# Kernel optimization log

Measured on AMD Instinct MI355X. Metric: run time of the kernel, lower is better.

Reference implementation:

```python
import jax, jax.numpy as jnp
import numpy as np


def lstm_cell(x, h, c, Wih, Whh, b):
    # PyTorch LSTM gate order: i, f, g, o
    z = x @ Wih.T + h @ Whh.T + b
    i, f, g, o = jnp.split(z, 4, axis=-1)
    c = jax.nn.sigmoid(f) * c + jax.nn.sigmoid(i) * jnp.tanh(g)
    h = jax.nn.sigmoid(o) * jnp.tanh(c)
    return h, c


def run_dir(xs, Wih, Whh, b, reverse):
    # xs: [S, B, D_in] -> outputs [S, B, H], final (h, c)
    B = xs.shape[1]
    H = Whh.shape[1]
    init = (jnp.zeros((B, H), xs.dtype), jnp.zeros((B, H), xs.dtype))
    def step(carry, x):
        h, c = carry
        h, c = lstm_cell(x, h, c, Wih, Whh, b)
        return (h, c), h
    (h, c), ys = jax.lax.scan(step, init, xs, reverse=reverse)
    return ys, h, c


def _p(k, shape, scale=0.05):
    return jax.random.normal(k, shape, dtype=jnp.float32) * scale


def setup_inputs():
    V, E, H = 32000, 128, 256
    B, S, T = 32, 256, 64
    ks = jax.random.split(jax.random.key(0), 24)
    return {
        "src": jax.random.randint(ks[0], (B, S), 0, V),
        "tgt": jax.random.randint(ks[1], (B, T), 0, V),
        "emb": _p(ks[2], (V, E), 1.0),
        "enc_Wih_l0": _p(ks[3], (2, 4 * H, E)),
        "enc_Whh_l0": _p(ks[4], (2, 4 * H, H)),
        "enc_b_l0": _p(ks[5], (2, 4 * H)),
        "enc_Wih_l1": _p(ks[6], (2, 4 * H, 2 * H)),
        "enc_Whh_l1": _p(ks[7], (2, 4 * H, H)),
        "enc_b_l1": _p(ks[8], (2, 4 * H)),
        "dec_Wih0": _p(ks[9], (8 * H, E + 2 * H)),
        "dec_Whh0": _p(ks[10], (8 * H, 2 * H)),
        "dec_b0": _p(ks[11], (8 * H,)),
        "dec_Wih1": _p(ks[12], (8 * H, 2 * H)),
        "dec_Whh1": _p(ks[13], (8 * H, 2 * H)),
        "dec_b1": _p(ks[14], (8 * H,)),
        "attn_W1": _p(ks[15], (H, 4 * H)),
        "attn_b1": _p(ks[16], (H,)),
        "attn_W2": _p(ks[17], (1, H)),
        "attn_b2": _p(ks[18], (1,)),
        "out_W1": _p(ks[19], (H, 2 * H)),
        "out_b1": _p(ks[20], (H,)),
        "out_W2": _p(ks[21], (V, H)),
        "out_b2": _p(ks[22], (V,)),
    }


def reference(src, tgt, emb, enc_Wih_l0, enc_Whh_l0, enc_b_l0, enc_Wih_l1, enc_Whh_l1, enc_b_l1, dec_Wih0, dec_Whh0, dec_b0, dec_Wih1, dec_Whh1, dec_b1, attn_W1, attn_b1, attn_W2, attn_b2, out_W1, out_b1, out_W2, out_b2):
    # dropout layers are identity in eval mode
    H2 = dec_Whh0.shape[1]  # 2*hidden_dim = 512
    src_e = emb[src]                        # [B, S, E]
    tgt_e = emb[tgt]                        # [B, T, E]
    xs = jnp.swapaxes(src_e, 0, 1)          # [S, B, E]

    # 2-layer bidirectional encoder
    yf, hf0, cf0 = run_dir(xs, enc_Wih_l0[0], enc_Whh_l0[0], enc_b_l0[0], False)
    yb, hb0, cb0 = run_dir(xs, enc_Wih_l0[1], enc_Whh_l0[1], enc_b_l0[1], True)
    y0 = jnp.concatenate([yf, yb], axis=-1)  # [S, B, 2H]
    yf1, hf1, cf1 = run_dir(y0, enc_Wih_l1[0], enc_Whh_l1[0], enc_b_l1[0], False)
    yb1, hb1, cb1 = run_dir(y0, enc_Wih_l1[1], enc_Whh_l1[1], enc_b_l1[1], True)
    enc_out = jnp.swapaxes(jnp.concatenate([yf1, yb1], axis=-1), 0, 1)  # [B, S, 2H]

    # decoder init: per-layer concat of fwd/bwd final states (matches the view/transpose)
    h0 = jnp.concatenate([hf0, hb0], axis=-1)
    c0 = jnp.concatenate([cf0, cb0], axis=-1)
    h1 = jnp.concatenate([hf1, hb1], axis=-1)
    c1 = jnp.concatenate([cf1, cb1], axis=-1)

    # attention: Linear(4H, H) split into decoder-hidden part and encoder part
    W1_dec = attn_W1[:, :H2]
    W1_enc = attn_W1[:, H2:]
    enc_proj = jnp.einsum('bsd,hd->bsh', enc_out, W1_enc) + attn_b1  # precompute once

    dec_xs = jnp.swapaxes(tgt_e[:, :-1, :], 0, 1)  # [T-1, B, E]

    def step(carry, x_t):
        h0, c0, h1, c1 = carry
        e = jnp.tanh(enc_proj + (h1 @ W1_dec.T)[:, None, :])  # [B, S, H]
        scores = e @ attn_W2[0] + attn_b2[0]                  # [B, S]
        a = jax.nn.softmax(scores, axis=1)
        ctx = jnp.einsum('bs,bsd->bd', a, enc_out)            # [B, 2H]
        x = jnp.concatenate([x_t, ctx], axis=-1)              # [B, E+2H]
        h0, c0 = lstm_cell(x, h0, c0, dec_Wih0, dec_Whh0, dec_b0)
        h1, c1 = lstm_cell(h0, h1, c1, dec_Wih1, dec_Whh1, dec_b1)
        hid = jax.nn.relu(h1 @ out_W1.T + out_b1)
        logits = hid @ out_W2.T + out_b2                      # [B, V]
        return (h0, c0, h1, c1), logits

    _, ys = jax.lax.scan(step, (h0, c0, h1, c1), dec_xs)      # [T-1, B, V]
    return jnp.swapaxes(ys, 0, 1)                             # [B, T-1, V]
```

## Files before the change

kernel.cpp:

```cpp
#include <hip/hip_runtime.h>

#define BB_ 32
#define SS_ 256
#define TD_ 63
#define EE_ 128
#define VV_ 32000

typedef unsigned short u16;
typedef unsigned int u32;
typedef unsigned long long u64;
typedef __attribute__((ext_vector_type(8))) short short8v;
typedef __attribute__((ext_vector_type(4))) float f32x4;

__device__ __forceinline__ float sigf(float x){ return 1.0f/(1.0f+__expf(-x)); }
__device__ __forceinline__ float tanhf_fast(float x){ return 1.0f - 2.0f/(__expf(2.0f*x)+1.0f); }
__device__ __forceinline__ u16 f2bf(float f){
  unsigned u = __float_as_uint(f);
  u += 0x7fff + ((u >> 16) & 1);
  return (u16)(u >> 16);
}
__device__ __forceinline__ u32 packbf(float a, float b){
  return (u32)f2bf(a) | ((u32)f2bf(b) << 16);
}
__device__ __forceinline__ float bflo(u32 v){ return __uint_as_float(v << 16); }
__device__ __forceinline__ float bfhi(u32 v){ return __uint_as_float(v & 0xffff0000u); }

__device__ __forceinline__ u32 aldu(const u32* p){
  return __hip_atomic_load(p, __ATOMIC_RELAXED, __HIP_MEMORY_SCOPE_AGENT);
}
__device__ __forceinline__ u64 ald64u(const u32* p){
  return __hip_atomic_load((const u64*)p, __ATOMIC_RELAXED, __HIP_MEMORY_SCOPE_AGENT);
}
__device__ __forceinline__ void astu(u32* p, u32 v){
  __hip_atomic_store(p, v, __ATOMIC_RELAXED, __HIP_MEMORY_SCOPE_AGENT);
}
__device__ __forceinline__ float aldf(const float* p){
  return __hip_atomic_load(p, __ATOMIC_RELAXED, __HIP_MEMORY_SCOPE_AGENT);
}
__device__ __forceinline__ void astf(float* p, float v){
  __hip_atomic_store(p, v, __ATOMIC_RELAXED, __HIP_MEMORY_SCOPE_AGENT);
}
__device__ __forceinline__ void vdrain(){ asm volatile("s_waitcnt vmcnt(0)" ::: "memory"); }

__device__ __forceinline__ short8v mkfrag(u64 a, u64 b){
  union { u32 u[4]; short8v v; } c;
  c.u[0] = (u32)a; c.u[1] = (u32)(a >> 32);
  c.u[2] = (u32)b; c.u[3] = (u32)(b >> 32);
  return c.v;
}

#define OFF_Z        0u
#define OFF_Y0       16777216u
#define OFF_Y1       20971520u
#define OFF_ZPRE     25165824u
#define OFF_H1ALL    29294592u
#define OFF_SRCE     30326784u
#define OFF_TGTE     31375360u
#define OFF_EPROJ    31633408u
#define OFF_ENCA0    33730560u
#define OFF_ENCA1    33992704u
#define OFF_DECA     34254848u
#define OFF_ATP      36352000u
#define OFF_E0H      36417536u
#define OFF_E0C      36433920u
#define OFF_E1H      36450304u
#define OFF_E1C      36466688u
#define OFF_H0P      36483072u
#define OFF_H1P      36499456u
#define OFF_CTXP     36515840u
#define OFF_CTXS     36532224u
#define OFF_Y1P      36532288u
#define OFF_HEXA     38629440u
#define OFF_HEXB     38645824u
#define OFF_BARS     38662208u

__device__ __forceinline__ void icbar(unsigned* ctr, unsigned target){
  vdrain();
  __syncthreads();
  if (threadIdx.x == 0){
    __hip_atomic_fetch_add(ctr, 1u, __ATOMIC_RELAXED, __HIP_MEMORY_SCOPE_AGENT);
    while (__hip_atomic_load(ctr, __ATOMIC_RELAXED, __HIP_MEMORY_SCOPE_AGENT) < target)
      __builtin_amdgcn_s_sleep(1);
  }
  __syncthreads();
  asm volatile("" ::: "memory");
}

__device__ __forceinline__ void icbar3(unsigned* db, unsigned gen, bool isRoot){
  vdrain();
  __syncthreads();
  int tid = threadIdx.x;
  unsigned g = (unsigned)blockIdx.x & 15u;
  if (tid == 0)
    __hip_atomic_fetch_add(&db[g*32], 1u, __ATOMIC_RELAXED, __HIP_MEMORY_SCOPE_AGENT);
  if (isRoot){
    if (tid < 64){
      unsigned tgt = gen * 8u;
      for (;;){
        unsigned a = (tid < 16)
          ? __hip_atomic_load(&db[(unsigned)tid*32], __ATOMIC_RELAXED, __HIP_MEMORY_SCOPE_AGENT)
          : tgt;
        if (__all(a >= tgt)) break;
        __builtin_amdgcn_s_sleep(1);
      }
      if (tid < 16)
        __hip_atomic_store(&db[512 + (unsigned)tid*32], gen, __ATOMIC_RELAXED, __HIP_MEMORY_SCOPE_AGENT);
    }
  } else {
    if (tid == 0){
      while (__hip_atomic_load(&db[512 + g*32], __ATOMIC_RELAXED, __HIP_MEMORY_SCOPE_AGENT) < gen)
        __builtin_amdgcn_s_sleep(1);
    }
  }
  __syncthreads();
  asm volatile("" ::: "memory");
}

__global__ void k_zero(float* __restrict__ p, int n){
  int i = blockIdx.x*256 + threadIdx.x;
  if (i < n) p[i] = 0.f;
}

__global__ void k_gather(const int* __restrict__ src, const int* __restrict__ tgt,
                         const float* __restrict__ emb,
                         float* __restrict__ src_e, float* __restrict__ tgt_e){
  int idx = blockIdx.x*256 + threadIdx.x;
  const int total = (8192 + 2016) * 32;
  if (idx >= total) return;
  int row = idx >> 5, j = idx & 31;
  int tok; float* dst;
  if (row < 8192){
    int s = row >> 5, b = row & 31;
    tok = src[b*SS_ + s];
    dst = src_e + (size_t)row*EE_;
  } else {
    int r2 = row - 8192;
    int t = r2 >> 5, b = r2 & 31;
    tok = tgt[b*64 + t];
    dst = tgt_e + (size_t)r2*EE_;
  }
  float4 v = *(const float4*)(emb + (size_t)tok*EE_ + j*4);
  *(float4*)(dst + j*4) = v;
}

__global__ void k_prep_encA(const float* __restrict__ W, u16* __restrict__ out){
  int idx = blockIdx.x*256 + threadIdx.x;
  if (idx >= 65536) return;
  int l = idx & 63, kk = (idx>>6)&7, m = (idx>>9)&7, us = (idx>>12)&7, d = (idx>>15)&1;
  int r = l & 15, g = r & 3, ut = r >> 2;
  int gcol = g*256 + us*32 + m*4 + ut;
  int k0 = kk*32 + (l>>4)*8;
  const float* wp = W + ((size_t)d*1024 + gcol)*256 + k0;
  u16 v[8];
  #pragma unroll
  for (int j=0;j<8;j++) v[j] = f2bf(wp[j]);
  *(uint4*)(out + (size_t)idx*8) = *(uint4*)v;
}

__global__ void k_prep_decA(const float* __restrict__ Wih0, const float* __restrict__ Whh0,
                            const float* __restrict__ Wih1, const float* __restrict__ Whh1,
                            u16* __restrict__ out){
  int idx = blockIdx.x*256 + threadIdx.x;
  if (idx >= 524288) return;
  int l = idx & 63, kk = (idx>>6)&31, cell = (idx>>11)&1, B = idx>>12;
  int r = l & 15;
  int ul = r >> 2, g = r & 3;
  int gcol = g*512 + B*4 + ul;
  int k0 = kk*32 + (l>>4)*8;
  u16 v[8];
  #pragma unroll
  for (int j=0;j<8;j++){
    int k = k0 + j;
    float wv;
    if (cell == 0) wv = (k < 512) ? Wih0[(size_t)gcol*640 + 128 + k] : Whh0[(size_t)gcol*512 + k - 512];
    else           wv = (k < 512) ? Wih1[(size_t)gcol*512 + k]       : Whh1[(size_t)gcol*512 + k - 512];
    v[j] = f2bf(wv);
  }
  *(uint4*)(out + (size_t)idx*8) = *(uint4*)v;
}

__global__ void k_prep_aTp(const float* __restrict__ aW1, u32* __restrict__ aTp){
  int idx = blockIdx.x*256 + threadIdx.x;
  if (idx >= 65536) return;
  int j2 = idx >> 8, c = idx & 255;
  aTp[idx] = packbf(aW1[(size_t)c*1024 + 2*j2], aW1[(size_t)c*1024 + 2*j2 + 1]);
}

__global__ void k_dinit(const float* __restrict__ eh0, const float* __restrict__ eh1,
                        u32* __restrict__ h0p, u32* __restrict__ h1p){
// ... 105 lines not shown
  unsigned* ctr = bars + dom*32;
  int w = tid >> 6, l = tid & 63;
  int lr = l & 15, lk = l >> 4;
  { const uint4* s = (const uint4*)(encA + (size_t)(d*8+us)*32768);
    uint4* dst = (uint4*)ldsA;
    for (int i = tid; i < 4096; i += 256) dst[i] = s[i]; }
  float c0 = 0.f, c1 = 0.f;
  int b_g = bh*16 + lr;
  int uc0 = us*32 + w*8 + lk, uc1 = uc0 + 4;
  u32* hx = hexp + dom*4096;
  __syncthreads();
  float za[4], zb[4];
  {
    int t0 = d ? 255 : 0;
    const float* zr = Z + ((size_t)t0*32 + b_g)*2048 + d*1024;
    #pragma unroll
    for (int j = 0; j < 4; j++){ za[j] = zr[j*256 + uc0]; zb[j] = zr[j*256 + uc1]; }
  }
  for (int i = 0; i < 256; i++){
    int t = d ? (255 - i) : i;
    int par_r = (i & 1) ^ 1;
    u64 bq[16];
    const u32* bs = hx + par_r*2048 + lr*128;
    #pragma unroll
    for (int kk = 0; kk < 8; kk++){
      bq[2*kk]   = ald64u(bs + kk*16 + lk*4);
      bq[2*kk+1] = ald64u(bs + kk*16 + lk*4 + 2);
    }
    f32x4 acc0 = (f32x4){0.f,0.f,0.f,0.f};
    f32x4 acc1 = (f32x4){0.f,0.f,0.f,0.f};
    #pragma unroll
    for (int kk = 0; kk < 8; kk++){
      short8v bF = mkfrag(bq[2*kk], bq[2*kk+1]);
      short8v a0 = *(const short8v*)(ldsA + (((w*2+0)*8 + kk)*64 + l)*16);
      short8v a1 = *(const short8v*)(ldsA + (((w*2+1)*8 + kk)*64 + l)*16);
      acc0 = __builtin_amdgcn_mfma_f32_16x16x32_bf16(a0, bF, acc0, 0, 0, 0);
      acc1 = __builtin_amdgcn_mfma_f32_16x16x32_bf16(a1, bF, acc1, 0, 0, 0);
    }
    float z0 = acc0[0]+za[0], z1 = acc0[1]+za[1], z2 = acc0[2]+za[2], z3 = acc0[3]+za[3];
    float cn = sigf(z1)*c0 + sigf(z0)*tanhf_fast(z2);
    float hn0 = sigf(z3)*tanhf_fast(cn); c0 = cn;
    z0 = acc1[0]+zb[0]; z1 = acc1[1]+zb[1]; z2 = acc1[2]+zb[2]; z3 = acc1[3]+zb[3];
    cn = sigf(z1)*c1 + sigf(z0)*tanhf_fast(z2);
    float hn1 = sigf(z3)*tanhf_fast(cn); c1 = cn;
    size_t yr = ((size_t)t*32 + b_g)*512 + d*256;
    y[yr + uc0] = hn0; y[yr + uc1] = hn1;
    float p0 = __shfl_xor(hn0, 16);
    float p1 = __shfl_xor(hn1, 16);
    if ((lk & 1) == 0){
      int base = us*16 + w*4 + (lk >> 1);
      u32 pk0 = packbf(hn0, p0), pk1 = packbf(hn1, p1);
      astu(hx + (i&1)*2048 + lr*128 + base,     pk0);
      astu(hx + (i&1)*2048 + lr*128 + base + 2, pk1);
      if (y1p){
        int gb = d*128 + base;
        y1p[((size_t)t*32 + b_g)*256 + gb]     = pk0;
        y1p[((size_t)t*32 + b_g)*256 + gb + 2] = pk1;
      }
    }
    if (i == 255){
      size_t fb = ((size_t)d*32 + b_g)*256;
      hfin[fb + uc0] = hn0; hfin[fb + uc1] = hn1;
      cfin[fb + uc0] = c0;  cfin[fb + uc1] = c1;
      break;
    }
    {
      int tn = d ? (254 - i) : (i + 1);
      const float* zr = Z + ((size_t)tn*32 + b_g)*2048 + d*1024;
      #pragma unroll
      for (int j = 0; j < 4; j++){ za[j] = zr[j*256 + uc0]; zb[j] = zr[j*256 + uc1]; }
    }
    icbar(ctr, (unsigned)(i+1)*8u);
  }
}

__global__ __launch_bounds__(256) void k_dec_scan(
    const u32* __restrict__ aTp, const float* __restrict__ eproj,
    const float* __restrict__ aW2, const u32* __restrict__ y1p,
    const float* __restrict__ zpre, const float* __restrict__ db1,
    const u16* __restrict__ decA,
    const float* __restrict__ e0c, const float* __restrict__ e1c,
    u32* __restrict__ h0p, u32* __restrict__ h1p,
    u32* __restrict__ ctxp, float* __restrict__ ctxS,
    float* __restrict__ H1all, unsigned* __restrict__ bars){
  extern __shared__ char smem[];
  char* ldsA = smem;
  f32x4* pAc0 = (f32x4*)(smem + 65536);
  f32x4* pAc1 = (f32x4*)(smem + 65536 + 2048);
  f32x4* pB   = (f32x4*)(smem + 65536 + 4096);
  f32x4* pC   = (f32x4*)(smem + 65536 + 6144);
  float* h1s = (float*)(smem + 65536 + 8192);
  float* qs  = h1s + 512;
  float* w2s = qs + 256;
  float* es  = w2s + 256;
  int Bid = blockIdx.x, tid = threadIdx.x;
  int w = tid >> 6, l = tid & 63;
  int n_ = w & 1, kh = w >> 1;
  int lr = l & 15, lk = l >> 4;
  int idx = n_*64 + l;
  bool isRoot = (Bid == 127);
  { const uint4* s = (const uint4*)(decA + (size_t)Bid*32768);
    uint4* d4 = (uint4*)ldsA;
    for (int i = tid; i < 4096; i += 256) d4[i] = s[i]; }
  bool att = (Bid < 64);
  int attb = Bid >> 1, attp = Bid & 1;
  if (att) w2s[tid] = aW2[tid];
  int u = Bid*4 + lk;
  int b_e = n_*16 + lr;
  float c0r=0.f, c1r=0.f, d0=0.f, d1=0.f, d2=0.f, d3=0.f;
  if (kh == 1){
    int dd = u >> 8, uu = u & 255;
    c0r = e0c[((size_t)dd*32 + b_e)*256 + uu];
    c1r = e1c[((size_t)dd*32 + b_e)*256 + uu];
    d0 = db1[u]; d1 = db1[512+u]; d2 = db1[1024+u]; d3 = db1[1536+u];
  }
  int brow_off = (n_*16 + lr)*256;
  __syncthreads();
  unsigned gen = 0;
  for (int t = 0; t < TD_; t++){
    int hp = t & 1;
    f32x4 rA0, rA1;
    float zp0=0.f, zp1=0.f, zp2=0.f, zp3=0.f;
    {
      if (kh == 1){
        const float* zp = zpre + ((size_t)t*32 + b_e)*2048 + u;
        zp0 = zp[0]; zp1 = zp[512]; zp2 = zp[1024]; zp3 = zp[1536];
      }
      const u32* r0 = h0p + hp*8192 + brow_off;
      const u32* r1 = h1p + hp*8192 + brow_off;
      u64 qa[16], qb[16];
      #pragma unroll
      for (int k2 = 0; k2 < 8; k2++){
        int a = (kh*8 + k2)*16 + lk*4;
        qa[2*k2] = ald64u(r0 + a); qa[2*k2+1] = ald64u(r0 + a + 2);
      }
      #pragma unroll
      for (int k2 = 0; k2 < 8; k2++){
        int a = (kh*8 + k2)*16 + lk*4;
        qb[2*k2] = ald64u(r1 + a); qb[2*k2+1] = ald64u(r1 + a + 2);
      }
      f32x4 aA = (f32x4){0.f,0.f,0.f,0.f};
      f32x4 aB = (f32x4){0.f,0.f,0.f,0.f};
      #pragma unroll
      for (int k2 = 0; k2 < 8; k2++){
        short8v aF = *(const short8v*)(ldsA + (((16 + kh*8 + k2)*64) + l)*16);
        aA = __builtin_amdgcn_mfma_f32_16x16x32_bf16(aF, mkfrag(qa[2*k2], qa[2*k2+1]), aA, 0, 0, 0);
      }
      #pragma unroll
      for (int k2 = 0; k2 < 8; k2++){
        short8v aF = *(const short8v*)(ldsA + (((48 + kh*8 + k2)*64) + l)*16);
        aB = __builtin_amdgcn_mfma_f32_16x16x32_bf16(aF, mkfrag(qb[2*k2], qb[2*k2+1]), aB, 0, 0, 0);
      }
      if (kh == 0){ pAc0[idx] = aA; pAc1[idx] = aB; }
      else        { rA0 = aA; rA1 = aB; }
    }
    if (att){
      int b = attb;
      u32 hv = aldu(h1p + hp*8192 + b*256 + tid);
      h1s[2*tid] = bflo(hv); h1s[2*tid+1] = bfhi(hv);
      __syncthreads();
      float q0=0.f,q1=0.f,q2=0.f,q3=0.f;
      for (int j2 = 0; j2 < 256; j2 += 4){
        u32 w0 = aTp[(j2+0)*256 + tid];
        u32 w1 = aTp[(j2+1)*256 + tid];
        u32 w2 = aTp[(j2+2)*256 + tid];
        u32 w3 = aTp[(j2+3)*256 + tid];
        q0 += bflo(w0)*h1s[2*j2]   + bfhi(w0)*h1s[2*j2+1];
        q1 += bflo(w1)*h1s[2*j2+2] + bfhi(w1)*h1s[2*j2+3];
        q2 += bflo(w2)*h1s[2*j2+4] + bfhi(w2)*h1s[2*j2+5];
        q3 += bflo(w3)*h1s[2*j2+6] + bfhi(w3)*h1s[2*j2+7];
      }
      qs[tid] = (q0+q1)+(q2+q3);
      __syncthreads();
      int sl = tid >> 3, hc = tid & 7;
      #pragma unroll
      for (int so = 0; so < 4; so++){
        int s = attp*128 + so*32 + sl;
        const float4* ep = (const float4*)(eproj + ((size_t)attb*256 + s)*256 + hc*32);
        const float4* q4 = (const float4*)(qs + hc*32);
        const float4* w4 = (const float4*)(w2s + hc*32);
        float acc = 0.f;
        #pragma unroll
        for (int k = 0; k < 8; k++){
          float4 e = ep[k], qq = q4[k], ww = w4[k];
          acc += tanhf_fast(e.x+qq.x)*ww.x + tanhf_fast(e.y+qq.y)*ww.y
               + tanhf_fast(e.z+qq.z)*ww.z + tanhf_fast(e.w+qq.w)*ww.w;
        }
        acc += __shfl_xor(acc, 1);
        acc += __shfl_xor(acc, 2);
        acc += __shfl_xor(acc, 4);
        if (hc == 0) es[so*32 + sl] = __expf(acc);
      }
      __syncthreads();
      float a0 = 0.f, a1 = 0.f, b0 = 0.f, b1 = 0.f, S = 0.f;
      size_t ybase = ((size_t)(attp*128)*32 + b)*256 + tid;
      #pragma unroll 8
      for (int si = 0; si < 128; si += 2){
        float e0 = es[si], e1 = es[si+1];
        u32 v0 = y1p[ybase + (size_t)si*8192];
        u32 v1 = y1p[ybase + (size_t)(si+1)*8192];
        S += e0 + e1;
        a0 += e0*bflo(v0); a1 += e0*bfhi(v0);
        b0 += e1*bflo(v1); b1 += e1*bfhi(v1);
      }
      astu(ctxp + attp*8192 + b*256 + tid, packbf(a0+b0, a1+b1));
      if (tid == 0) astf(ctxS + attp*32 + b, S);
    }
    icbar3(bars, ++gen, isRoot);
    {
      float Sa = 0.f, Sb = 0.f;
      if (kh == 1){ Sa = aldf(ctxS + b_e); Sb = aldf(ctxS + 32 + b_e); }
      const u32* rc = ctxp + kh*8192 + brow_off;
      u64 qc[32];
      #pragma unroll
      for (int kk = 0; kk < 16; kk++){
        int a = kk*16 + lk*4;
        qc[2*kk] = ald64u(rc + a); qc[2*kk+1] = ald64u(rc + a + 2);
      }
      f32x4 acc = (f32x4){0.f,0.f,0.f,0.f};
      #pragma unroll
      for (int kk = 0; kk < 16; kk++){
        short8v aF = *(const short8v*)(ldsA + ((kk*64) + l)*16);
        acc = __builtin_amdgcn_mfma_f32_16x16x32_bf16(aF, mkfrag(qc[2*kk], qc[2*kk+1]), acc, 0, 0, 0);
      }
      if (kh == 0) pB[idx] = acc;
      __syncthreads();
      if (kh == 1){
        f32x4 oc = pB[idx];
        f32x4 oh = pAc0[idx];
        float sc = 1.0f / (Sa + Sb);
        float z0 = (acc[0]+oc[0])*sc + oh[0] + rA0[0] + zp0;
        float z1 = (acc[1]+oc[1])*sc + oh[1] + rA0[1] + zp1;
        float z2 = (acc[2]+oc[2])*sc + oh[2] + rA0[2] + zp2;
        float z3 = (acc[3]+oc[3])*sc + oh[3] + rA0[3] + zp3;
        float cn = sigf(z1)*c0r + sigf(z0)*tanhf_fast(z2);
        float hn = sigf(z3)*tanhf_fast(cn);
        c0r = cn;
        float other = __shfl_xor(hn, 16);
        if ((lk & 1) == 0)
          astu(h0p + (1-hp)*8192 + b_e*256 + Bid*2 + (lk>>1), packbf(hn, other));
      }
    }
    icbar3(bars, ++gen, isRoot);
    {
      const u32* rh = h0p + (1-hp)*8192 + brow_off;
      u64 qd[16];
      #pragma unroll
      for (int k2 = 0; k2 < 8; k2++){
        int a = (kh*8 + k2)*16 + lk*4;
        qd[2*k2] = ald64u(rh + a); qd[2*k2+1] = ald64u(rh + a + 2);
      }
      f32x4 acc = (f32x4){0.f,0.f,0.f,0.f};
      #pragma unroll
      for (int k2 = 0; k2 < 8; k2++){
        short8v aF = *(const short8v*)(ldsA + (((32 + kh*8 + k2)*64) + l)*16);
        acc = __builtin_amdgcn_mfma_f32_16x16x32_bf16(aF, mkfrag(qd[2*k2], qd[2*k2+1]), acc, 0, 0, 0);
      }
      if (kh == 0) pC[idx] = acc;
      __syncthreads();
      if (kh == 1){
        f32x4 oc = pC[idx];
        f32x4 oh = pAc1[idx];
        float z0 = acc[0] + oc[0] + oh[0] + rA1[0] + d0;
        float z1 = acc[1] + oc[1] + oh[1] + rA1[1] + d1;
        float z2 = acc[2] + oc[2] + oh[2] + rA1[2] + d2;
        float z3 = acc[3] + oc[3] + oh[3] + rA1[3] + d3;
        float cn = sigf(z1)*c1r + sigf(z0)*tanhf_fast(z2);
        float hn = sigf(z3)*tanhf_fast(cn);
        c1r = cn;
        H1all[((size_t)t*32 + b_e)*512 + u] = hn;
        float other = __shfl_xor(hn, 16);
        if ((lk & 1) == 0)
          astu(h1p + (1-hp)*8192 + b_e*256 + Bid*2 + (lk>>1), packbf(hn, other));
      }
    }
    if (t < TD_-1) icbar3(bars, ++gen, isRoot);
  }
}

extern "C" void kernel_launch(void* const* d_in, const int* in_sizes, int n_in,
                              void* d_out, int out_size, void* d_ws, size_t ws_size,
                              hipStream_t stream){
  (void)in_sizes; (void)n_in; (void)out_size; (void)ws_size;
  const int*   src   = (const int*)d_in[0];
  const int*   tgt   = (const int*)d_in[1];
  const float* emb   = (const float*)d_in[2];
  const float* eWih0 = (const float*)d_in[3];
  const float* eWhh0 = (const float*)d_in[4];
  const float* eb0   = (const float*)d_in[5];
  const float* eWih1 = (const float*)d_in[6];
  const float* eWhh1 = (const float*)d_in[7];
  const float* eb1   = (const float*)d_in[8];
  const float* dWih0 = (const float*)d_in[9];
  const float* dWhh0 = (const float*)d_in[10];
  const float* db0   = (const float*)d_in[11];
  const float* dWih1 = (const float*)d_in[12];
  const float* dWhh1 = (const float*)d_in[13];
  const float* db1   = (const float*)d_in[14];
  const float* aW1   = (const float*)d_in[15];
  const float* ab1   = (const float*)d_in[16];
  const float* aW2   = (const float*)d_in[17];
  const float* oW1   = (const float*)d_in[19];
  const float* ob1   = (const float*)d_in[20];
  const float* oW2   = (const float*)d_in[21];
  const float* ob2   = (const float*)d_in[22];

  float* F = (float*)d_out;
  float* Z     = F + OFF_Z;
  float* y0    = F + OFF_Y0;
  float* y1    = F + OFF_Y1;
  float* zpre  = F + OFF_ZPRE;
  float* H1    = F + OFF_H1ALL;
  float* srcE  = F + OFF_SRCE;
  float* tgtE  = F + OFF_TGTE;
  float* eproj = F + OFF_EPROJ;
  u16*   encA0 = (u16*)(F + OFF_ENCA0);
  u16*   encA1 = (u16*)(F + OFF_ENCA1);
  u16*   decA  = (u16*)(F + OFF_DECA);
  u32*   aTp   = (u32*)(F + OFF_ATP);
  float* e0h   = F + OFF_E0H;
  float* e0c   = F + OFF_E0C;
  float* e1h   = F + OFF_E1H;
  float* e1c   = F + OFF_E1C;
  u32*   h0p   = (u32*)(F + OFF_H0P);
  u32*   h1p   = (u32*)(F + OFF_H1P);
  u32*   ctxp  = (u32*)(F + OFF_CTXP);
  float* ctxS  = F + OFF_CTXS;
  u32*   y1p   = (u32*)(F + OFF_Y1P);
  u32*   hexA  = (u32*)(F + OFF_HEXA);
  u32*   hexB  = (u32*)(F + OFF_HEXB);
  unsigned* bars = (unsigned*)(F + OFF_BARS);
  float* hid   = (float*)d_ws;

  hipFuncSetAttribute((const void*)k_enc_scan, hipFuncAttributeMaxDynamicSharedMemorySize, 65536);
  hipFuncSetAttribute((const void*)k_dec_scan, hipFuncAttributeMaxDynamicSharedMemorySize, 78336);

  k_zero<<<135,256,0,stream>>>(F + OFF_HEXA, 34304);
  k_gather<<<((8192+2016)*32+255)/256,256,0,stream>>>(src, tgt, emb, srcE, tgtE);
  k_prep_encA<<<256,256,0,stream>>>(eWhh0, encA0);
  k_prep_encA<<<256,256,0,stream>>>(eWhh1, encA1);
  k_prep_decA<<<2048,256,0,stream>>>(dWih0, dWhh0, dWih1, dWhh1, decA);
  k_prep_aTp<<<256,256,0,stream>>>(aW1, aTp);

  k_mgemm<<<dim3(64,16),256,0,stream>>>(srcE, eWih0, eb0, Z, 8192,2048,128, 128,0,0);
  k_enc_scan<<<32,256,65536,stream>>>(Z, encA0, y0, (u32*)nullptr, hexA, e0h, e0c, bars);
  k_mgemm<<<dim3(64,16),256,0,stream>>>(y0, eWih1, eb1, Z, 8192,2048,512, 512,0,0);
  k_enc_scan<<<32,256,65536,stream>>>(Z, encA1, y1, y1p, hexB, e1h, e1c, bars + 128);

  k_mgemm<<<dim3(64,2),256,0,stream>>>(y1, aW1, ab1, eproj, 8192,256,512, 1024,512,4);
  k_mgemm<<<dim3(16,16),256,0,stream>>>(tgtE, dWih0, db0, zpre, 2016,2048,128, 640,0,0);
  k_dinit<<<32,256,0,stream>>>(e0h, e1h, h0p, h1p);

  k_dec_scan<<<128,256,78336,stream>>>(aTp, eproj, aW2, y1p, zpre, db1, decA,
                                       e0c, e1c, h0p, h1p, ctxp, ctxS, H1, bars + 256);

  k_mgemm<<<dim3(16,2),256,0,stream>>>(H1, oW1, ob1, hid, 2016,256,512, 512,0,1);
  k_mgemm<<<dim3(16,250),256,0,stream>>>(hid, oW2, ob2, F, 2016,32000,256, 256,0,2);
}
```

Before: 4.504 ms.

## Overlap output projection GEMMs with decoder scan using extra consumer blocks

The decoder scan kernel is launched with 128 extra blocks when the workspace is large enough. These blocks compute the hidden ReLU projection and the vocab-logits GEMM on 4-timestep chunks of H1 as soon as the scan's barrier generation counter shows those chunks are finished. This hides the two separate post-scan GEMM launches behind the latency-bound recurrence. Decoder buffers move to the workspace, and the root block publishes a global generation counter. In exchange, the consumer blocks compete with the scan blocks for memory bandwidth and L2, and correctness relies on all 256 blocks being co-resident.

```diff
diff --git a/kernel.cpp b/kernel.cpp
--- a/kernel.cpp
+++ b/kernel.cpp
@@ -74,6 +74,20 @@
 #define OFF_HEXB     38645824u
 #define OFF_BARS     38662208u
 
+#define W_EPROJ   0u
+#define W_ZPRE    2097152u
+#define W_Y1P     6225920u
+#define W_DECA    8323072u
+#define W_ATP     10420224u
+#define W_H0P     10485760u
+#define W_H1P     10502144u
+#define W_CTXP    10518528u
+#define W_CTXS    10534912u
+#define W_H1ALL   10534976u
+#define W_HIDP    11567168u
+#define W_DBAR    11829312u
+#define W_TOTAL   11831360u
+
 __device__ __forceinline__ void icbar(unsigned* ctr, unsigned target){
   vdrain();
   __syncthreads();
@@ -105,6 +119,8 @@
       }
       if (tid < 16)
         __hip_atomic_store(&db[512 + (unsigned)tid*32], gen, __ATOMIC_RELAXED, __HIP_MEMORY_SCOPE_AGENT);
+      if (tid == 16)
+        __hip_atomic_store(&db[1024], gen, __ATOMIC_RELAXED, __HIP_MEMORY_SCOPE_AGENT);
     }
   } else {
     if (tid == 0){
@@ -376,206 +392,371 @@
     const float* __restrict__ e0c, const float* __restrict__ e1c,
     u32* __restrict__ h0p, u32* __restrict__ h1p,
     u32* __restrict__ ctxp, float* __restrict__ ctxS,
-    float* __restrict__ H1all, unsigned* __restrict__ bars){
+    float* __restrict__ H1all, unsigned* __restrict__ bars,
+    const float* __restrict__ oW1, const float* __restrict__ ob1,
+    const float* __restrict__ oW2, const float* __restrict__ ob2,
+    u32* __restrict__ hidp, float* __restrict__ out){
   extern __shared__ char smem[];
-  char* ldsA = smem;
-  f32x4* pAc0 = (f32x4*)(smem + 65536);
-  f32x4* pAc1 = (f32x4*)(smem + 65536 + 2048);
-  f32x4* pB   = (f32x4*)(smem + 65536 + 4096);
-  f32x4* pC   = (f32x4*)(smem + 65536 + 6144);
-  float* h1s = (float*)(smem + 65536 + 8192);
-  float* qs  = h1s + 512;
-  float* w2s = qs + 256;
-  float* es  = w2s + 256;
   int Bid = blockIdx.x, tid = threadIdx.x;
-  int w = tid >> 6, l = tid & 63;
-  int n_ = w & 1, kh = w >> 1;
-  int lr = l & 15, lk = l >> 4;
-  int idx = n_*64 + l;
-  bool isRoot = (Bid == 127);
-  { const uint4* s = (const uint4*)(decA + (size_t)Bid*32768);
-    uint4* d4 = (uint4*)ldsA;
-    for (int i = tid; i < 4096; i += 256) d4[i] = s[i]; }
-  bool att = (Bid < 64);
-  int attb = Bid >> 1, attp = Bid & 1;
-  if (att) w2s[tid] = aW2[tid];
-  int u = Bid*4 + lk;
-  int b_e = n_*16 + lr;
-  float c0r=0.f, c1r=0.f, d0=0.f, d1=0.f, d2=0.f, d3=0.f;
-  if (kh == 1){
-    int dd = u >> 8, uu = u & 255;
-    c0r = e0c[((size_t)dd*32 + b_e)*256 + uu];
-    c1r = e1c[((size_t)dd*32 + b_e)*256 + uu];
-    d0 = db1[u]; d1 = db1[512+u]; d2 = db1[1024+u]; d3 = db1[1536+u];
-  }
-  int brow_off = (n_*16 + lr)*256;
-  __syncthreads();
-  unsigned gen = 0;
-  for (int t = 0; t < TD_; t++){
-    int hp = t & 1;
-    f32x4 rA0, rA1;
-    float zp0=0.f, zp1=0.f, zp2=0.f, zp3=0.f;
-    {
-      if (kh == 1){
-        const float* zp = zpre + ((size_t)t*32 + b_e)*2048 + u;
-        zp0 = zp[0]; zp1 = zp[512]; zp2 = zp[1024]; zp3 = zp[1536];
-      }
-      const u32* r0 = h0p + hp*8192 + brow_off;
-      const u32* r1 = h1p + hp*8192 + brow_off;
-      u64 qa[16], qb[16];
+
+  if (Bid < 128){
+    char* ldsA = smem;
+    f32x4* pAc0 = (f32x4*)(smem + 65536);
+    f32x4* pAc1 = (f32x4*)(smem + 65536 + 2048);
+    f32x4* pB   = (f32x4*)(smem + 65536 + 4096);
+    f32x4* pC   = (f32x4*)(smem + 65536 + 6144);
+    float* h1s = (float*)(smem + 65536 + 8192);
+    float* qs  = h1s + 512;
+    float* w2s = qs + 256;
+    float* es  = w2s + 256;
+    int w = tid >> 6, l = tid & 63;
+    int n_ = w & 1, kh = w >> 1;
+    int lr = l & 15, lk = l >> 4;
+    int idx = n_*64 + l;
+    bool isRoot = (Bid == 127);
+    { const uint4* s = (const uint4*)(decA + (size_t)Bid*32768);
+      uint4* d4 = (uint4*)ldsA;
+      for (int i = tid; i < 4096; i += 256) d4[i] = s[i]; }
+    bool att = (Bid < 64);
+    int attb = Bid >> 1, attp = Bid & 1;
+    if (att) w2s[tid] = aW2[tid];
+    int u = Bid*4 + lk;
+    int b_e = n_*16 + lr;
+    float c0r=0.f, c1r=0.f, d0=0.f, d1=0.f, d2=0.f, d3=0.f;
+    if (kh == 1){
+      int dd = u >> 8, uu = u & 255;
+      c0r = e0c[((size_t)dd*32 + b_e)*256 + uu];
+      c1r = e1c[((size_t)dd*32 + b_e)*256 + uu];
+      d0 = db1[u]; d1 = db1[512+u]; d2 = db1[1024+u]; d3 = db1[1536+u];
+    }
+    int brow_off = (n_*16 + lr)*256;
+    __syncthreads();
+    unsigned gen = 0;
+    for (int t = 0; t < TD_; t++){
+      int hp = t & 1;
+      f32x4 rA0, rA1;
+      float zp0=0.f, zp1=0.f, zp2=0.f, zp3=0.f;
+      {
+        if (kh == 1){
+          const float* zp = zpre + ((size_t)t*32 + b_e)*2048 + u;
+          zp0 = zp[0]; zp1 = zp[512]; zp2 = zp[1024]; zp3 = zp[1536];
+        }
+        const u32* r0 = h0p + hp*8192 + brow_off;
+        const u32* r1 = h1p + hp*8192 + brow_off;
+        u64 qa[16], qb[16];
+        #pragma unroll
+        for (int k2 = 0; k2 < 8; k2++){
+          int a = (kh*8 + k2)*16 + lk*4;
+          qa[2*k2] = ald64u(r0 + a); qa[2*k2+1] = ald64u(r0 + a + 2);
+        }
+        #pragma unroll
+        for (int k2 = 0; k2 < 8; k2++){
+          int a = (kh*8 + k2)*16 + lk*4;
+          qb[2*k2] = ald64u(r1 + a); qb[2*k2+1] = ald64u(r1 + a + 2);
+        }
+        f32x4 aA = (f32x4){0.f,0.f,0.f,0.f};
+        f32x4 aB = (f32x4){0.f,0.f,0.f,0.f};
+        #pragma unroll
+        for (int k2 = 0; k2 < 8; k2++){
+          short8v aF = *(const short8v*)(ldsA + (((16 + kh*8 + k2)*64) + l)*16);
+          aA = __builtin_amdgcn_mfma_f32_16x16x32_bf16(aF, mkfrag(qa[2*k2], qa[2*k2+1]), aA, 0, 0, 0);
+        }
+        #pragma unroll
+        for (int k2 = 0; k2 < 8; k2++){
+          short8v aF = *(const short8v*)(ldsA + (((48 + kh*8 + k2)*64) + l)*16);
+          aB = __builtin_amdgcn_mfma_f32_16x16x32_bf16(aF, mkfrag(qb[2*k2], qb[2*k2+1]), aB, 0, 0, 0);
+        }
+        if (kh == 0){ pAc0[idx] = aA; pAc1[idx] = aB; }
+        else        { rA0 = aA; rA1 = aB; }
+      }
+      if (att){
+        int b = attb;
+        u32 hv = aldu(h1p + hp*8192 + b*256 + tid);
+        h1s[2*tid] = bflo(hv); h1s[2*tid+1] = bfhi(hv);
+        __syncthreads();
+        float q0=0.f,q1=0.f,q2=0.f,q3=0.f;
+        for (int j2 = 0; j2 < 256; j2 += 4){
+          u32 w0 = aTp[(j2+0)*256 + tid];
+          u32 w1 = aTp[(j2+1)*256 + tid];
+          u32 w2 = aTp[(j2+2)*256 + tid];
+          u32 w3 = aTp[(j2+3)*256 + tid];
+          q0 += bflo(w0)*h1s[2*j2]   + bfhi(w0)*h1s[2*j2+1];
+          q1 += bflo(w1)*h1s[2*j2+2] + bfhi(w1)*h1s[2*j2+3];
+          q2 += bflo(w2)*h1s[2*j2+4] + bfhi(w2)*h1s[2*j2+5];
+          q3 += bflo(w3)*h1s[2*j2+6] + bfhi(w3)*h1s[2*j2+7];
+        }
+        qs[tid] = (q0+q1)+(q2+q3);
+        __syncthreads();
+        int sl = tid >> 3, hc = tid & 7;
+        #pragma unroll
+        for (int so = 0; so < 4; so++){
+          int s = attp*128 + so*32 + sl;
+          const float4* ep = (const float4*)(eproj + ((size_t)attb*256 + s)*256 + hc*32);
+          const float4* q4 = (const float4*)(qs + hc*32);
+          const float4* w4 = (const float4*)(w2s + hc*32);
+          float acc = 0.f;
+          #pragma unroll
+          for (int k = 0; k < 8; k++){
+            float4 e = ep[k], qq = q4[k], ww = w4[k];
+            acc += tanhf_fast(e.x+qq.x)*ww.x + tanhf_fast(e.y+qq.y)*ww.y
+                 + tanhf_fast(e.z+qq.z)*ww.z + tanhf_fast(e.w+qq.w)*ww.w;
+          }
+          acc += __shfl_xor(acc, 1);
+          acc += __shfl_xor(acc, 2);
+          acc += __shfl_xor(acc, 4);
+          if (hc == 0) es[so*32 + sl] = __expf(acc);
+        }
+        __syncthreads();
+        float a0 = 0.f, a1 = 0.f, b0 = 0.f, b1 = 0.f, S = 0.f;
+        size_t ybase = ((size_t)(attp*128)*32 + b)*256 + tid;
+        #pragma unroll 8
+        for (int si = 0; si < 128; si += 2){
+          float e0 = es[si], e1 = es[si+1];
+          u32 v0 = y1p[ybase + (size_t)si*8192];
+          u32 v1 = y1p[ybase + (size_t)(si+1)*8192];
+          S += e0 + e1;
+          a0 += e0*bflo(v0); a1 += e0*bfhi(v0);
+          b0 += e1*bflo(v1); b1 += e1*bfhi(v1);
+        }
+        astu(ctxp + attp*8192 + b*256 + tid, packbf(a0+b0, a1+b1));
+        if (tid == 0) astf(ctxS + attp*32 + b, S);
+      }
+      icbar3(bars, ++gen, isRoot);
+      {
+        float Sa = 0.f, Sb = 0.f;
+        if (kh == 1){ Sa = aldf(ctxS + b_e); Sb = aldf(ctxS + 32 + b_e); }
+        const u32* rc = ctxp + kh*8192 + brow_off;
+        u64 qc[32];
+        #pragma unroll
+        for (int kk = 0; kk < 16; kk++){
+          int a = kk*16 + lk*4;
+          qc[2*kk] = ald64u(rc + a); qc[2*kk+1] = ald64u(rc + a + 2);
+        }
+        f32x4 acc = (f32x4){0.f,0.f,0.f,0.f};
+        #pragma unroll
+        for (int kk = 0; kk < 16; kk++){
+          short8v aF = *(const short8v*)(ldsA + ((kk*64) + l)*16);
+          acc = __builtin_amdgcn_mfma_f32_16x16x32_bf16(aF, mkfrag(qc[2*kk], qc[2*kk+1]), acc, 0, 0, 0);
+        }
+        if (kh == 0) pB[idx] = acc;
+        __syncthreads();
+        if (kh == 1){
+          f32x4 oc = pB[idx];
+          f32x4 oh = pAc0[idx];
+          float sc = 1.0f / (Sa + Sb);
+          float z0 = (acc[0]+oc[0])*sc + oh[0] + rA0[0] + zp0;
+          float z1 = (acc[1]+oc[1])*sc + oh[1] + rA0[1] + zp1;
+          float z2 = (acc[2]+oc[2])*sc + oh[2] + rA0[2] + zp2;
+          float z3 = (acc[3]+oc[3])*sc + oh[3] + rA0[3] + zp3;
+          float cn = sigf(z1)*c0r + sigf(z0)*tanhf_fast(z2);
+          float hn = sigf(z3)*tanhf_fast(cn);
+          c0r = cn;
+          float other = __shfl_xor(hn, 16);
+          if ((lk & 1) == 0)
+            astu(h0p + (1-hp)*8192 + b_e*256 + Bid*2 + (lk>>1), packbf(hn, other));
+        }
+      }
+      icbar3(bars, ++gen, isRoot);
+      {
+        const u32* rh = h0p + (1-hp)*8192 + brow_off;
+        u64 qd[16];
+        #pragma unroll
+        for (int k2 = 0; k2 < 8; k2++){
+          int a = (kh*8 + k2)*16 + lk*4;
+          qd[2*k2] = ald64u(rh + a); qd[2*k2+1] = ald64u(rh + a + 2);
+        }
+        f32x4 acc = (f32x4){0.f,0.f,0.f,0.f};
+        #pragma unroll
+        for (int k2 = 0; k2 < 8; k2++){
+          short8v aF = *(const short8v*)(ldsA + (((32 + kh*8 + k2)*64) + l)*16);
+          acc = __builtin_amdgcn_mfma_f32_16x16x32_bf16(aF, mkfrag(qd[2*k2], qd[2*k2+1]), acc, 0, 0, 0);
+        }
+        if (kh == 0) pC[idx] = acc;
+        __syncthreads();
+        if (kh == 1){
+          f32x4 oc = pC[idx];
+          f32x4 oh = pAc1[idx];
+          float z0 = acc[0] + oc[0] + oh[0] + rA1[0] + d0;
+          float z1 = acc[1] + oc[1] + oh[1] + rA1[1] + d1;
+          float z2 = acc[2] + oc[2] + oh[2] + rA1[2] + d2;
+          float z3 = acc[3] + oc[3] + oh[3] + rA1[3] + d3;
+          float cn = sigf(z1)*c1r + sigf(z0)*tanhf_fast(z2);
+          float hn = sigf(z3)*tanhf_fast(cn);
+          c1r = cn;
+          astf(&H1all[((size_t)t*32 + b_e)*512 + u], hn);
+          float other = __shfl_xor(hn, 16);
+          if ((lk & 1) == 0)
+            astu(h1p + (1-hp)*8192 + b_e*256 + Bid*2 + (lk>>1), packbf(hn, other));
+        }
+      }
+      icbar3(bars, ++gen, isRoot);
+    }
+  } else {
+    u16* As = (u16*)smem;
+    u16* Bs = (u16*)(smem + 128*72*2);
+    int hb = Bid - 128;
+    int l = tid & 63, w = tid >> 6;
+    int wr = w >> 1, wc = w & 1;
+    int lr16 = l & 15, lk8 = (l >> 4) * 8;
+    int r = tid >> 1, half = tid & 1;
+    int cp = ((hb & 7) == 0 && (hb >> 3) < 16) ? (hb >> 3) : -1;
+    for (int j = hb; j < 4000; j += 128){
+      int c = j / 250, n = j % 250;
+      if (cp >= 0 && cp <= c){
+        unsigned need = (cp == 15) ? 189u : (unsigned)(12*cp + 12);
+        if (tid == 0){
+          while (aldu(bars + 1024) < need) __builtin_amdgcn_s_sleep(32);
+        }
+        __syncthreads();
+        int rows = (cp == 15) ? 96 : 128;
+        const float* Hc = H1all + (size_t)cp*128*512;
+        for (int n0 = 0; n0 < 256; n0 += 128){
+          f32x4 acc[4][4];
+          #pragma unroll
+          for (int m=0;m<4;m++)
+            #pragma unroll
+            for (int nn=0;nn<4;nn++) acc[m][nn] = (f32x4){0.f,0.f,0.f,0.f};
+          for (int k0 = 0; k0 < 512; k0 += 64){
+            u16* asd = &As[r*72 + half*32];
+            if (r < rows){
+              const u32* ap = (const u32*)(Hc + (size_t)r*512 + k0 + half*32);
+              #pragma unroll
+              for (int jj = 0; jj < 16; jj++){
+                u64 v2 = ald64u(ap + 2*jj);
+                asd[2*jj]   = f2bf(__uint_as_float((u32)v2));
+                asd[2*jj+1] = f2bf(__uint_as_float((u32)(v2>>32)));
+              }
+            } else {
+              #pragma unroll
+              for (int jj = 0; jj < 16; jj++){ asd[2*jj]=0; asd[2*jj+1]=0; }
+            }
+            const float* brow = oW1 + (size_t)(n0 + r)*512 + k0 + half*32;
+            u16* bsd = &Bs[r*72 + half*32];
+            #pragma unroll
+            for (int jj = 0; jj < 4; jj++){
+              float4 p = *(const float4*)(brow + jj*8);
+              float4 q = *(const float4*)(brow + jj*8 + 4);
+              bsd[jj*8+0]=f2bf(p.x); bsd[jj*8+1]=f2bf(p.y); bsd[jj*8+2]=f2bf(p.z); bsd[jj*8+3]=f2bf(p.w);
+              bsd[jj*8+4]=f2bf(q.x); bsd[jj*8+5]=f2bf(q.y); bsd[jj*8+6]=f2bf(q.z); bsd[jj*8+7]=f2bf(q.w);
+            }
+            __syncthreads();
+            #pragma unroll
+            for (int kk = 0; kk < 2; kk++){
+              short8v aF[4], bF[4];
+              #pragma unroll
+              for (int m = 0; m < 4; m++)
+                aF[m] = *(short8v*)&As[(wr*64 + m*16 + lr16)*72 + kk*32 + lk8];
+              #pragma unroll
+              for (int nn = 0; nn < 4; nn++)
+                bF[nn] = *(short8v*)&Bs[(wc*64 + nn*16 + lr16)*72 + kk*32 + lk8];
+              #pragma unroll
+              for (int m = 0; m < 4; m++)
+                #pragma unroll
+                for (int nn = 0; nn < 4; nn++)
+                  acc[m][nn] = __builtin_amdgcn_mfma_f32_16x16x32_bf16(aF[m], bF[nn], acc[m][nn], 0, 0, 0);
+            }
+            __syncthreads();
+          }
+          #pragma unroll
+          for (int m = 0; m < 4; m++){
+            int gr0 = wr*64 + m*16 + (l >> 4)*4;
+            #pragma unroll
+            for (int nn = 0; nn < 4; nn++){
+              int gc = n0 + wc*64 + nn*16 + (l & 15);
+              float bv = ob1[gc];
+              #pragma unroll
+              for (int j4 = 0; j4 < 4; j4++){
+                int gr = gr0 + j4;
+                float v = fmaxf(acc[m][nn][j4] + bv, 0.f);
+                float o = __shfl_xor(v, 1);
+                if ((l & 1) == 0 && gr < rows)
+                  astu(hidp + (size_t)cp*16384 + gr*128 + (gc>>1), packbf(v, o));
+              }
+            }
+          }
+        }
+        vdrain();
+        __syncthreads();
+        if (tid == 0) astu(bars + 1088 + cp, 1u);
+        cp = -1;
+      }
+      if (tid == 0){
+        while (aldu(bars + 1088 + c) == 0) __builtin_amdgcn_s_sleep(16);
+      }
+      __syncthreads();
+      int rows = (c == 15) ? 96 : 128;
+      int n0g = n * 128;
+      f32x4 acc[4][4];
       #pragma unroll
-      for (int k2 = 0; k2 < 8; k2++){
-        int a = (kh*8 + k2)*16 + lk*4;
-        qa[2*k2] = ald64u(r0 + a); qa[2*k2+1] = ald64u(r0 + a + 2);
+      for (int m=0;m<4;m++)
+        #pragma unroll
+        for (int nn=0;nn<4;nn++) acc[m][nn] = (f32x4){0.f,0.f,0.f,0.f};
+      const u32* hc = hidp + (size_t)c*16384;
+      for (int k0 = 0; k0 < 256; k0 += 64){
+        u32* asd32 = (u32*)&As[r*72 + half*32];
+        if (r < rows){
+          const u32* ap = hc + r*128 + (k0>>1) + half*16;
+          #pragma unroll
+          for (int jj = 0; jj < 8; jj++){
+            u64 v2 = ald64u(ap + 2*jj);
+            asd32[2*jj] = (u32)v2; asd32[2*jj+1] = (u32)(v2>>32);
+          }
+        } else {
+          #pragma unroll
+          for (int jj = 0; jj < 8; jj++){ asd32[2*jj]=0; asd32[2*jj+1]=0; }
+        }
+        const float* brow = oW2 + (size_t)(n0g + r)*256 + k0 + half*32;
+        u16* bsd = &Bs[r*72 + half*32];
+        #pragma unroll
+        for (int jj = 0; jj < 4; jj++){
+          float4 p = *(const float4*)(brow + jj*8);
+          float4 q = *(const float4*)(brow + jj*8 + 4);
+          bsd[jj*8+0]=f2bf(p.x); bsd[jj*8+1]=f2bf(p.y); bsd[jj*8+2]=f2bf(p.z); bsd[jj*8+3]=f2bf(p.w);
+          bsd[jj*8+4]=f2bf(q.x); bsd[jj*8+5]=f2bf(q.y); bsd[jj*8+6]=f2bf(q.z); bsd[jj*8+7]=f2bf(q.w);
+        }
+        __syncthreads();
+        #pragma unroll
+        for (int kk = 0; kk < 2; kk++){
+          short8v aF[4], bF[4];
+          #pragma unroll
+          for (int m = 0; m < 4; m++)
+            aF[m] = *(short8v*)&As[(wr*64 + m*16 + lr16)*72 + kk*32 + lk8];
+          #pragma unroll
+          for (int nn = 0; nn < 4; nn++)
+            bF[nn] = *(short8v*)&Bs[(wc*64 + nn*16 + lr16)*72 + kk*32 + lk8];
+          #pragma unroll
+          for (int m = 0; m < 4; m++)
+            #pragma unroll
+            for (int nn = 0; nn < 4; nn++)
+              acc[m][nn] = __builtin_amdgcn_mfma_f32_16x16x32_bf16(aF[m], bF[nn], acc[m][nn], 0, 0, 0);
+        }
+        __syncthreads();
       }
       #pragma unroll
-      for (int k2 = 0; k2 < 8; k2++){
-        int a = (kh*8 + k2)*16 + lk*4;
-        qb[2*k2] = ald64u(r1 + a); qb[2*k2+1] = ald64u(r1 + a + 2);
-      }
-      f32x4 aA = (f32x4){0.f,0.f,0.f,0.f};
-      f32x4 aB = (f32x4){0.f,0.f,0.f,0.f};
-      #pragma unroll
-      for (int k2 = 0; k2 < 8; k2++){
-        short8v aF = *(const short8v*)(ldsA + (((16 + kh*8 + k2)*64) + l)*16);
-        aA = __builtin_amdgcn_mfma_f32_16x16x32_bf16(aF, mkfrag(qa[2*k2], qa[2*k2+1]), aA, 0, 0, 0);
-      }
-      #pragma unroll
-      for (int k2 = 0; k2 < 8; k2++){
-        short8v aF = *(const short8v*)(ldsA + (((48 + kh*8 + k2)*64) + l)*16);
-        aB = __builtin_amdgcn_mfma_f32_16x16x32_bf16(aF, mkfrag(qb[2*k2], qb[2*k2+1]), aB, 0, 0, 0);
-      }
-      if (kh == 0){ pAc0[idx] = aA; pAc1[idx] = aB; }
-      else        { rA0 = aA; rA1 = aB; }
-    }
-    if (att){
-      int b = attb;
-      u32 hv = aldu(h1p + hp*8192 + b*256 + tid);
-      h1s[2*tid] = bflo(hv); h1s[2*tid+1] = bfhi(hv);
-      __syncthreads();
-      float q0=0.f,q1=0.f,q2=0.f,q3=0.f;
-      for (int j2 = 0; j2 < 256; j2 += 4){
-        u32 w0 = aTp[(j2+0)*256 + tid];
-        u32 w1 = aTp[(j2+1)*256 + tid];
-        u32 w2 = aTp[(j2+2)*256 + tid];
-        u32 w3 = aTp[(j2+3)*256 + tid];
-        q0 += bflo(w0)*h1s[2*j2]   + bfhi(w0)*h1s[2*j2+1];
-        q1 += bflo(w1)*h1s[2*j2+2] + bfhi(w1)*h1s[2*j2+3];
-        q2 += bflo(w2)*h1s[2*j2+4] + bfhi(w2)*h1s[2*j2+5];
-        q3 += bflo(w3)*h1s[2*j2+6] + bfhi(w3)*h1s[2*j2+7];
-      }
-      qs[tid] = (q0+q1)+(q2+q3);
-      __syncthreads();
-      int sl = tid >> 3, hc = tid & 7;
-      #pragma unroll
-      for (int so = 0; so < 4; so++){
-        int s = attp*128 + so*32 + sl;
-        const float4* ep = (const float4*)(eproj + ((size_t)attb*256 + s)*256 + hc*32);
-        const float4* q4 = (const float4*)(qs + hc*32);
-        const float4* w4 = (const float4*)(w2s + hc*32);
-        float acc = 0.f;
-        #pragma unroll
-        for (int k = 0; k < 8; k++){
-          float4 e = ep[k], qq = q4[k], ww = w4[k];
-          acc += tanhf_fast(e.x+qq.x)*ww.x + tanhf_fast(e.y+qq.y)*ww.y
-               + tanhf_fast(e.z+qq.z)*ww.z + tanhf_fast(e.w+qq.w)*ww.w;
-        }
-        acc += __shfl_xor(acc, 1);
-        acc += __shfl_xor(acc, 2);
-        acc += __shfl_xor(acc, 4);
-        if (hc == 0) es[so*32 + sl] = __expf(acc);
-      }
-      __syncthreads();
-      float a0 = 0.f, a1 = 0.f, b0 = 0.f, b1 = 0.f, S = 0.f;
-      size_t ybase = ((size_t)(attp*128)*32 + b)*256 + tid;
-      #pragma unroll 8
-      for (int si = 0; si < 128; si += 2){
-        float e0 = es[si], e1 = es[si+1];
-        u32 v0 = y1p[ybase + (size_t)si*8192];
-        u32 v1 = y1p[ybase + (size_t)(si+1)*8192];
-        S += e0 + e1;
-        a0 += e0*bflo(v0); a1 += e0*bfhi(v0);
-        b0 += e1*bflo(v1); b1 += e1*bfhi(v1);
-      }
-      astu(ctxp + attp*8192 + b*256 + tid, packbf(a0+b0, a1+b1));
-      if (tid == 0) astf(ctxS + attp*32 + b, S);
-    }
-    icbar3(bars, ++gen, isRoot);
-    {
-      float Sa = 0.f, Sb = 0.f;
-      if (kh == 1){ Sa = aldf(ctxS + b_e); Sb = aldf(ctxS + 32 + b_e); }
-      const u32* rc = ctxp + kh*8192 + brow_off;
-      u64 qc[32];
-      #pragma unroll
-      for (int kk = 0; kk < 16; kk++){
-        int a = kk*16 + lk*4;
-        qc[2*kk] = ald64u(rc + a); qc[2*kk+1] = ald64u(rc + a + 2);
-      }
-      f32x4 acc = (f32x4){0.f,0.f,0.f,0.f};
-      #pragma unroll
-      for (int kk = 0; kk < 16; kk++){
-        short8v aF = *(const short8v*)(ldsA + ((kk*64) + l)*16);
-        acc = __builtin_amdgcn_mfma_f32_16x16x32_bf16(aF, mkfrag(qc[2*kk], qc[2*kk+1]), acc, 0, 0, 0);
-      }
-      if (kh == 0) pB[idx] = acc;
-      __syncthreads();
-      if (kh == 1){
-        f32x4 oc = pB[idx];
-        f32x4 oh = pAc0[idx];
-        float sc = 1.0f / (Sa + Sb);
-        float z0 = (acc[0]+oc[0])*sc + oh[0] + rA0[0] + zp0;
-        float z1 = (acc[1]+oc[1])*sc + oh[1] + rA0[1] + zp1;
-        float z2 = (acc[2]+oc[2])*sc + oh[2] + rA0[2] + zp2;
-        float z3 = (acc[3]+oc[3])*sc + oh[3] + rA0[3] + zp3;
-        float cn = sigf(z1)*c0r + sigf(z0)*tanhf_fast(z2);
-        float hn = sigf(z3)*tanhf_fast(cn);
-        c0r = cn;
-        float other = __shfl_xor(hn, 16);
-        if ((lk & 1) == 0)
-          astu(h0p + (1-hp)*8192 + b_e*256 + Bid*2 + (lk>>1), packbf(hn, other));
-      }
-    }
-    icbar3(bars, ++gen, isRoot);
-    {
-      const u32* rh = h0p + (1-hp)*8192 + brow_off;
-      u64 qd[16];
-      #pragma unroll
-      for (int k2 = 0; k2 < 8; k2++){
-        int a = (kh*8 + k2)*16 + lk*4;
-        qd[2*k2] = ald64u(rh + a); qd[2*k2+1] = ald64u(rh + a + 2);
-      }
-      f32x4 acc = (f32x4){0.f,0.f,0.f,0.f};
-      #pragma unroll
-      for (int k2 = 0; k2 < 8; k2++){
-        short8v aF = *(const short8v*)(ldsA + (((32 + kh*8 + k2)*64) + l)*16);
-        acc = __builtin_amdgcn_mfma_f32_16x16x32_bf16(aF, mkfrag(qd[2*k2], qd[2*k2+1]), acc, 0, 0, 0);
-      }
-      if (kh == 0) pC[idx] = acc;
-      __syncthreads();
-      if (kh == 1){
-        f32x4 oc = pC[idx];
-        f32x4 oh = pAc1[idx];
-        float z0 = acc[0] + oc[0] + oh[0] + rA1[0] + d0;
-        float z1 = acc[1] + oc[1] + oh[1] + rA1[1] + d1;
-        float z2 = acc[2] + oc[2] + oh[2] + rA1[2] + d2;
-        float z3 = acc[3] + oc[3] + oh[3] + rA1[3] + d3;
-        float cn = sigf(z1)*c1r + sigf(z0)*tanhf_fast(z2);
-        float hn = sigf(z3)*tanhf_fast(cn);
-        c1r = cn;
-        H1all[((size_t)t*32 + b_e)*512 + u] = hn;
-        float other = __shfl_xor(hn, 16);
-        if ((lk & 1) == 0)
-          astu(h1p + (1-hp)*8192 + b_e*256 + Bid*2 + (lk>>1), packbf(hn, other));
-      }
-    }
-    if (t < TD_-1) icbar3(bars, ++gen, isRoot);
+      for (int m = 0; m < 4; m++){
+        int gr0 = wr*64 + m*16 + (l >> 4)*4;
+        #pragma unroll
+        for (int nn = 0; nn < 4; nn++){
+          int gc = n0g + wc*64 + nn*16 + (l & 15);
+          float bv = ob2[gc];
+          #pragma unroll
+          for (int j4 = 0; j4 < 4; j4++){
+            int gr = gr0 + j4;
+            if (gr < rows){
+              int gt = c*4 + (gr >> 5), b = gr & 31;
+              out[((size_t)(b*63 + gt))*(size_t)VV_ + gc] = acc[m][nn][j4] + bv;
+            }
+          }
+        }
+      }
+    }
   }
 }
 
 extern "C" void kernel_launch(void* const* d_in, const int* in_sizes, int n_in,
                               void* d_out, int out_size, void* d_ws, size_t ws_size,
                               hipStream_t stream){
-  (void)in_sizes; (void)n_in; (void)out_size; (void)ws_size;
+  (void)in_sizes; (void)n_in; (void)out_size;
   const int*   src   = (const int*)d_in[0];
   const int*   tgt   = (const int*)d_in[1];
   const float* emb   = (const float*)d_in[2];
@@ -600,36 +781,43 @@
   const float* ob2   = (const float*)d_in[22];
 
   float* F = (float*)d_out;
+  float* W = (float*)d_ws;
+  bool fused = (ws_size >= (size_t)48*1024*1024);
+
   float* Z     = F + OFF_Z;
   float* y0    = F + OFF_Y0;
   float* y1    = F + OFF_Y1;
-  float* zpre  = F + OFF_ZPRE;
-  float* H1    = F + OFF_H1ALL;
   float* srcE  = F + OFF_SRCE;
   float* tgtE  = F + OFF_TGTE;
-  float* eproj = F + OFF_EPROJ;
   u16*   encA0 = (u16*)(F + OFF_ENCA0);
   u16*   encA1 = (u16*)(F + OFF_ENCA1);
-  u16*   decA  = (u16*)(F + OFF_DECA);
-  u32*   aTp   = (u32*)(F + OFF_ATP);
   float* e0h   = F + OFF_E0H;
   float* e0c   = F + OFF_E0C;
   float* e1h   = F + OFF_E1H;
   float* e1c   = F + OFF_E1C;
-  u32*   h0p   = (u32*)(F + OFF_H0P);
-  u32*   h1p   = (u32*)(F + OFF_H1P);
-  u32*   ctxp  = (u32*)(F + OFF_CTXP);
-  float* ctxS  = F + OFF_CTXS;
-  u32*   y1p   = (u32*)(F + OFF_Y1P);
   u32*   hexA  = (u32*)(F + OFF_HEXA);
   u32*   hexB  = (u32*)(F + OFF_HEXB);
   unsigned* bars = (unsigned*)(F + OFF_BARS);
+
+  float* zpre  = fused ? (W + W_ZPRE)  : (F + OFF_ZPRE);
+  float* H1    = fused ? (W + W_H1ALL) : (F + OFF_H1ALL);
+  float* eproj = fused ? (W + W_EPROJ) : (F + OFF_EPROJ);
+  u16*   decA  = fused ? (u16*)(W + W_DECA) : (u16*)(F + OFF_DECA);
+  u32*   aTp   = fused ? (u32*)(W + W_ATP)  : (u32*)(F + OFF_ATP);
+  u32*   h0p   = fused ? (u32*)(W + W_H0P)  : (u32*)(F + OFF_H0P);
+  u32*   h1p   = fused ? (u32*)(W + W_H1P)  : (u32*)(F + OFF_H1P);
+  u32*   ctxp  = fused ? (u32*)(W + W_CTXP) : (u32*)(F + OFF_CTXP);
+  float* ctxS  = fused ? (W + W_CTXS)       : (F + OFF_CTXS);
+  u32*   y1p   = fused ? (u32*)(W + W_Y1P)  : (u32*)(F + OFF_Y1P);
+  unsigned* dbars = fused ? (unsigned*)(W + W_DBAR) : (bars + 256);
+  u32*   hidp  = fused ? (u32*)(W + W_HIDP) : (u32*)d_ws;
   float* hid   = (float*)d_ws;
 
   hipFuncSetAttribute((const void*)k_enc_scan, hipFuncAttributeMaxDynamicSharedMemorySize, 65536);
   hipFuncSetAttribute((const void*)k_dec_scan, hipFuncAttributeMaxDynamicSharedMemorySize, 78336);
 
   k_zero<<<135,256,0,stream>>>(F + OFF_HEXA, 34304);
+  if (fused) k_zero<<<8,256,0,stream>>>(W + W_DBAR, 2048);
   k_gather<<<((8192+2016)*32+255)/256,256,0,stream>>>(src, tgt, emb, srcE, tgtE);
   k_prep_encA<<<256,256,0,stream>>>(eWhh0, encA0);
   k_prep_encA<<<256,256,0,stream>>>(eWhh1, encA1);
@@ -645,9 +833,13 @@
   k_mgemm<<<dim3(16,16),256,0,stream>>>(tgtE, dWih0, db0, zpre, 2016,2048,128, 640,0,0);
   k_dinit<<<32,256,0,stream>>>(e0h, e1h, h0p, h1p);
 
-  k_dec_scan<<<128,256,78336,stream>>>(aTp, eproj, aW2, y1p, zpre, db1, decA,
-                                       e0c, e1c, h0p, h1p, ctxp, ctxS, H1, bars + 256);
-
-  k_mgemm<<<dim3(16,2),256,0,stream>>>(H1, oW1, ob1, hid, 2016,256,512, 512,0,1);
-  k_mgemm<<<dim3(16,250),256,0,stream>>>(hid, oW2, ob2, F, 2016,32000,256, 256,0,2);
-}
+  int decBlocks = fused ? 256 : 128;
+  k_dec_scan<<<decBlocks,256,78336,stream>>>(aTp, eproj, aW2, y1p, zpre, db1, decA,
+                                             e0c, e1c, h0p, h1p, ctxp, ctxS, H1, dbars,
+                                             oW1, ob1, oW2, ob2, hidp, F);
+
+  if (!fused){
+    k_mgemm<<<dim3(16,2),256,0,stream>>>(H1, oW1, ob1, hid, 2016,256,512, 512,0,1);
+    k_mgemm<<<dim3(16,250),256,0,stream>>>(hid, oW2, ob2, F, 2016,32000,256, 256,0,2);
+  }
+}
```

Result: no change. 4.473 ms (-0.7%).
